# Kernel tuning notes

Measured on AMD Instinct MI355X. Metric: run time of the kernel, lower is better.

Reference implementation:

```python
import jax, jax.numpy as jnp
import numpy as np

LEAKY_SLOPE = 0.2
EPS = 1e-16


def setup_inputs() -> dict:
    key = jax.random.key(0)
    k1, k2, k3, k4, k5 = jax.random.split(key, 5)
    N, E, IN, H, C = 50000, 800000, 128, 4, 16
    x = jax.random.normal(k1, (N, IN), dtype=jnp.float32)
    edge_index = jax.random.randint(k2, (2, E), 0, N, dtype=jnp.int64)
    # xavier_uniform-ish init, gain folded in as plain normal scale for a correctness baseline
    W = jax.random.normal(k3, (IN, H * C), dtype=jnp.float32) * (1.414 * (6.0 / (IN + H * C)) ** 0.5)
    a_src = jax.random.normal(k4, (1, H, C), dtype=jnp.float32) * 0.3
    a_dst = jax.random.normal(k5, (1, H, C), dtype=jnp.float32) * 0.3
    bias = jnp.zeros((H * C,), dtype=jnp.float32)
    return {"x": x, "edge_index": edge_index, "W": W, "a_src": a_src, "a_dst": a_dst, "bias": bias}


def reference(x, edge_index, W, a_src, a_dst, bias):
    N = x.shape[0]
    H, C = a_src.shape[1], a_src.shape[2]
    h = (x @ W).reshape(N, H, C)                      # [N, H, C]
    src, dst = edge_index[0], edge_index[1]
    alpha_src = (h * a_src).sum(-1)                    # [N, H]
    alpha_dst = (h * a_dst).sum(-1)                    # [N, H]
    alpha = alpha_src[src] + alpha_dst[dst]            # [E, H]
    alpha = jnp.where(alpha >= 0, alpha, LEAKY_SLOPE * alpha)
    # segment softmax over edges grouped by dst
    max_per = jax.ops.segment_max(alpha, dst, num_segments=N)  # [N, H], -inf for empty
    max_per = jnp.where(jnp.isinf(max_per), jnp.zeros_like(max_per), max_per)
    exp_s = jnp.exp(alpha - max_per[dst])              # [E, H]
    denom = jax.ops.segment_sum(exp_s, dst, num_segments=N)
    denom = jnp.maximum(denom, EPS)
    attn = exp_s / denom[dst]                          # [E, H]
    msg = h[src] * attn[..., None]                     # [E, H, C]
    out = jax.ops.segment_sum(msg, dst, num_segments=N)  # [N, H, C]
    out = out.reshape(N, H * C) + bias                 # concat=True
    return out
```

## Files before the change

kernel.cpp:

```cpp
#include <hip/hip_runtime.h>

#define LEAKY 0.2f
#define EPSV 1e-16f

constexpr int N_IN = 128;
constexpr int HC   = 64;
constexpr int H    = 4;
constexpr int CAP  = 48;
constexpr int LDK  = 136;
constexpr int SH   = 6;
constexpr int BNODES = 64;
constexpr int NBK  = 782;
constexpr int BCAP = 1344;
constexpr int CHUNK = 2048;

typedef __attribute__((ext_vector_type(8))) short bf16x8;
typedef __attribute__((ext_vector_type(4))) float f32x4;

__device__ __forceinline__ unsigned short bf16_rne(float f) {
    unsigned int b = __float_as_uint(f);
    return (unsigned short)((b + 0x7fffu + ((b >> 16) & 1u)) >> 16);
}

__global__ __launch_bounds__(256) void gemm_bin_fused(
        const float* __restrict__ x,
        const float* __restrict__ W,
        const float* __restrict__ a_src,
        const float* __restrict__ a_dst,
        const int* __restrict__ src,
        const int* __restrict__ dst,
        unsigned short* __restrict__ h_bf,
        float* __restrict__ as_out,
        float* __restrict__ ad_out,
        unsigned int* __restrict__ binned,
        int* __restrict__ bcursor,
        int N, int E, int gb) {
    __shared__ __align__(16) char smem[2 * 64 * LDK * sizeof(unsigned short)];
    int t = threadIdx.x;

    if (blockIdx.x >= gb) {
        int* hist  = (int*)smem;
        int* run   = hist + NBK;
        int* basep = run + NBK;
        for (int i = t; i < NBK; i += 256) { hist[i] = 0; run[i] = 0; }
        __syncthreads();

        int e0 = (blockIdx.x - gb) * CHUNK;
        int myb[8]; unsigned int myv[8];
        #pragma unroll
        for (int i = 0; i < 8; ++i) {
            int e = e0 + i * 256 + t;
            if (e < E) {
                int s = src[e], d = dst[e];
                myb[i] = d >> SH;
                myv[i] = ((unsigned int)(d & (BNODES - 1)) << 16) | (unsigned int)s;
                atomicAdd(&hist[myb[i]], 1);
            } else myb[i] = -1;
        }
        __syncthreads();

        for (int i = t; i < NBK; i += 256) {
            int h = hist[i];
            basep[i] = h ? atomicAdd(&bcursor[i], h) : 0;
        }
        __syncthreads();

        #pragma unroll
        for (int i = 0; i < 8; ++i) {
            int b = myb[i];
            if (b >= 0) {
                int r = atomicAdd(&run[b], 1);
                int g = basep[b] + r;
                if (g < BCAP) binned[b * BCAP + g] = myv[i];
            }
        }
        return;
    }

    unsigned short* xt = (unsigned short*)smem;
    unsigned short* wt = xt + 64 * LDK;
    int rowbase_blk = blockIdx.x * 64;

    #pragma unroll
    for (int i = 0; i < 32; ++i) {
        int idx = i * 256 + t;
        int k = idx >> 6, c = idx & 63;
        wt[c * LDK + k] = bf16_rne(W[idx]);
    }

    #pragma unroll
    for (int i = 0; i < 8; ++i) {
        int f = i * 256 + t;
        int row = f >> 5;
        int f4  = f & 31;
        int g = rowbase_blk + row;
        float4 v = (g < N) ? ((const float4*)x)[(size_t)g * 32 + f4]
                           : make_float4(0.f, 0.f, 0.f, 0.f);
        ushort4 pv;
        pv.x = bf16_rne(v.x); pv.y = bf16_rne(v.y);
        pv.z = bf16_rne(v.z); pv.w = bf16_rne(v.w);
        *(ushort4*)&xt[row * LDK + f4 * 4] = pv;
    }
    __syncthreads();

    int w = t >> 6, l = t & 63;
    int cl = l & 15;
    int rg = (l >> 4) * 4;

    f32x4 acc[4] = {{0,0,0,0},{0,0,0,0},{0,0,0,0},{0,0,0,0}};

    const int arow = w * 16 + cl;
    const int koff = (l >> 4) * 8;
    #pragma unroll
    for (int kk = 0; kk < 4; ++kk) {
        bf16x8 af = *(const bf16x8*)&xt[arow * LDK + kk * 32 + koff];
        #pragma unroll
        for (int c = 0; c < 4; ++c) {
            bf16x8 bfr = *(const bf16x8*)&wt[(c * 16 + cl) * LDK + kk * 32 + koff];
            acc[c] = __builtin_amdgcn_mfma_f32_16x16x32_bf16(af, bfr, acc[c], 0, 0, 0);
        }
    }

    float asv[4], adv[4];
    #pragma unroll
    for (int c = 0; c < 4; ++c) {
        asv[c] = a_src[c * 16 + cl];
        adv[c] = a_dst[c * 16 + cl];
    }

    float as_rc[4][4], ad_rc[4][4];
    #pragma unroll
    for (int c = 0; c < 4; ++c) {
        #pragma unroll
        for (int r = 0; r < 4; ++r) {
            float v = acc[c][r];
            int g = rowbase_blk + w * 16 + rg + r;
            if (g < N) h_bf[(size_t)g * HC + c * 16 + cl] = bf16_rne(v);
            as_rc[r][c] = v * asv[c];
            ad_rc[r][c] = v * adv[c];
        }
    }

    #pragma unroll
    for (int off = 1; off < 16; off <<= 1) {
        #pragma unroll
        for (int r = 0; r < 4; ++r)
            #pragma unroll
            for (int c = 0; c < 4; ++c) {
                as_rc[r][c] += __shfl_xor(as_rc[r][c], off, 64);
                ad_rc[r][c] += __shfl_xor(ad_rc[r][c], off, 64);
            }
    }

    #pragma unroll
    for (int r = 0; r < 4; ++r)
        #pragma unroll
        for (int c = 0; c < 4; ++c) {
            if (cl == r * 4 + c) {
                int g = rowbase_blk + w * 16 + rg + r;
                if (g < N) {
                    as_out[g * H + c] = as_rc[r][c];
                    ad_out[g * H + c] = ad_rc[r][c];
                }
            }
        }
}

__global__ __launch_bounds__(512) void agg_fused(
        const unsigned int* __restrict__ binned, const int* __restrict__ bcursor,
        const unsigned short* __restrict__ h_bf,
        const float* __restrict__ as_in, const float* __restrict__ ad_in,
        const float* __restrict__ bias,
        float* __restrict__ out, int N) {
    __shared__ int cnt[BNODES];
    __shared__ unsigned short lists[BNODES * CAP];
    int b = blockIdx.x, t = threadIdx.x;
    if (t < BNODES) cnt[t] = 0;
    __syncthreads();

    int ne = min(bcursor[b], BCAP);
    const unsigned int* bp = binned + (size_t)b * BCAP;
    for (int i = t; i < ne; i += 512) {
        unsigned int p = bp[i];
        int dl = p >> 16;
        int s  = p & 0xffff;
        int r = atomicAdd(&cnt[dl], 1);
        if (r < CAP) lists[dl * CAP + r] = (unsigned short)s;
    }
    __syncthreads();

    int dl = t >> 3;
    int l8 = t & 7;
    int hh = l8 >> 1;
    const uint4* hp4 = (const uint4*)h_bf;

    int wid = b * BNODES + dl;
    if (wid >= N) return;

    float4 bvlo = ((const float4*)bias)[2 * l8];
    float4 bvhi = ((const float4*)bias)[2 * l8 + 1];

    int deg = min(cnt[dl], CAP);
    float ad_d = ad_in[wid * H + hh];

    float a0 = 0.f, a1 = 0.f, a2 = 0.f, a3 = 0.f;
    float a4 = 0.f, a5 = 0.f, a6 = 0.f, a7 = 0.f;
    float dn = 0.f;

    for (int j = 0; j < deg; j += 4) {
        int ss[4]; float aa[4]; uint4 hv[4];
        #pragma unroll
        for (int k = 0; k < 4; ++k)
            ss[k] = (j + k < deg) ? (int)lists[dl * CAP + j + k] : 0;
        #pragma unroll
        for (int k = 0; k < 4; ++k) {
            aa[k] = as_in[ss[k] * H + hh];
            hv[k] = hp4[(size_t)ss[k] * 8 + l8];
        }
        #pragma unroll
        for (int k = 0; k < 4; ++k) {
            float a = aa[k] + ad_d;
            a = (a >= 0.f) ? a : LEAKY * a;
            float wgt = ((j + k) < deg) ? __expf(a) : 0.f;
            dn += wgt;
            a0 = fmaf(wgt, __uint_as_float(hv[k].x << 16),          a0);
            a1 = fmaf(wgt, __uint_as_float(hv[k].x & 0xffff0000u), a1);
            a2 = fmaf(wgt, __uint_as_float(hv[k].y << 16),          a2);
            a3 = fmaf(wgt, __uint_as_float(hv[k].y & 0xffff0000u), a3);
            a4 = fmaf(wgt, __uint_as_float(hv[k].z << 16),          a4);
            a5 = fmaf(wgt, __uint_as_float(hv[k].z & 0xffff0000u), a5);
            a6 = fmaf(wgt, __uint_as_float(hv[k].w << 16),          a6);
            a7 = fmaf(wgt, __uint_as_float(hv[k].w & 0xffff0000u), a7);
        }
    }

    float inv = 1.f / fmaxf(dn, EPSV);
    float4 olo, ohi;
    olo.x = a0 * inv + bvlo.x;
    olo.y = a1 * inv + bvlo.y;
    olo.z = a2 * inv + bvlo.z;
    olo.w = a3 * inv + bvlo.w;
    ohi.x = a4 * inv + bvhi.x;
    ohi.y = a5 * inv + bvhi.y;
    ohi.z = a6 * inv + bvhi.z;
    ohi.w = a7 * inv + bvhi.w;
    ((float4*)out)[(size_t)wid * 16 + 2 * l8]     = olo;
    ((float4*)out)[(size_t)wid * 16 + 2 * l8 + 1] = ohi;
}

extern "C" void kernel_launch(void* const* d_in, const int* in_sizes, int n_in,
                              void* d_out, int out_size, void* d_ws, size_t ws_size,
                              hipStream_t stream) {
    const float* x     = (const float*)d_in[0];
    const int*   ei    = (const int*)d_in[1];
    const float* W     = (const float*)d_in[2];
    const float* a_src = (const float*)d_in[3];
    const float* a_dst = (const float*)d_in[4];
    const float* bias  = (const float*)d_in[5];

    int N = in_sizes[0] / N_IN;
    int E = in_sizes[1] / 2;
    const int* src = ei;
    const int* dst = ei + E;

    float* out = (float*)d_out;

    unsigned short* h_bf = (unsigned short*)d_ws;
    float* as_buf = (float*)(h_bf + (size_t)N * HC);
    float* ad_buf = as_buf + (size_t)N * H;
    unsigned int* binned = (unsigned int*)(ad_buf + (size_t)N * H);
    int* bcursor  = (int*)(binned + (size_t)NBK * BCAP);

    hipMemsetAsync(bcursor, 0, NBK * sizeof(int), stream);

    int gb = (N + 63) / 64;
    int bb = (E + CHUNK - 1) / CHUNK;
    gemm_bin_fused<<<gb + bb, 256, 0, stream>>>(
        x, W, a_src, a_dst, src, dst, h_bf, as_buf, ad_buf, binned, bcursor, N, E, gb);

    agg_fused<<<NBK, 512, 0, stream>>>(
        binned, bcursor, h_bf, as_buf, ad_buf, bias, out, N);
}
```

Measured before the change: 54.40 us.

## Replace global atomic bin cursors with per-chunk local sort and offset table

The edge binning pass no longer reserves slots in fixed-capacity global bins through global atomics. Each chunk block now prefix-scans its local histogram, sorts its edges by bucket into shared memory, writes them out contiguously, and records per-bucket offsets in a transposed table. The aggregation kernel then gathers each bucket's edges by having one thread walk each chunk's slice. This removes the memset, the global atomics and the BCAP overflow truncation. In exchange the agg kernel makes about 391 small serial scattered reads per block, which may be slower than the old contiguous bin read.

```diff
diff --git a/kernel.cpp b/kernel.cpp
--- a/kernel.cpp
+++ b/kernel.cpp
@@ -11,7 +11,7 @@
 constexpr int SH   = 6;
 constexpr int BNODES = 64;
 constexpr int NBK  = 782;
-constexpr int BCAP = 1344;
+constexpr int NBK1 = 783;
 constexpr int CHUNK = 2048;
 
 typedef __attribute__((ext_vector_type(8))) short bf16x8;
@@ -33,19 +33,24 @@
         float* __restrict__ as_out,
         float* __restrict__ ad_out,
         unsigned int* __restrict__ binned,
-        int* __restrict__ bcursor,
+        unsigned short* __restrict__ offT,
         int N, int E, int gb) {
     __shared__ __align__(16) char smem[2 * 64 * LDK * sizeof(unsigned short)];
     int t = threadIdx.x;
 
     if (blockIdx.x >= gb) {
-        int* hist  = (int*)smem;
-        int* run   = hist + NBK;
-        int* basep = run + NBK;
-        for (int i = t; i < NBK; i += 256) { hist[i] = 0; run[i] = 0; }
-        __syncthreads();
-
-        int e0 = (blockIdx.x - gb) * CHUNK;
+        int* hist = (int*)smem;
+        int* pref = hist + 1024;
+        int* run  = pref + 1024;
+        int* wsum = run + 784;
+        unsigned int* stage = (unsigned int*)(wsum + 256);
+
+        for (int i = t; i < 1024; i += 256) { hist[i] = 0; pref[i] = 0; }
+        for (int i = t; i < 784; i += 256) run[i] = 0;
+        __syncthreads();
+
+        int blk = blockIdx.x - gb;
+        int e0 = blk * CHUNK;
         int myb[8]; unsigned int myv[8];
         #pragma unroll
         for (int i = 0; i < 8; ++i) {
@@ -59,21 +64,42 @@
         }
         __syncthreads();
 
-        for (int i = t; i < NBK; i += 256) {
-            int h = hist[i];
-            basep[i] = h ? atomicAdd(&bcursor[i], h) : 0;
-        }
-        __syncthreads();
+        int s4 = 0;
+        #pragma unroll
+        for (int j = 0; j < 4; ++j) s4 += hist[t * 4 + j];
+        wsum[t] = s4;
+        for (int off = 1; off < 256; off <<= 1) {
+            __syncthreads();
+            int add = (t >= off) ? wsum[t - off] : 0;
+            __syncthreads();
+            wsum[t] += add;
+        }
+        __syncthreads();
+        int running = wsum[t] - s4;
+        #pragma unroll
+        for (int j = 0; j < 4; ++j) {
+            int e = t * 4 + j;
+            if (e < NBK1) pref[e] = running;
+            running += hist[e];
+        }
+        __syncthreads();
+
+        for (int e = t; e < NBK1; e += 256)
+            offT[(size_t)blk * NBK1 + e] = (unsigned short)pref[e];
 
         #pragma unroll
         for (int i = 0; i < 8; ++i) {
             int b = myb[i];
             if (b >= 0) {
                 int r = atomicAdd(&run[b], 1);
-                int g = basep[b] + r;
-                if (g < BCAP) binned[b * BCAP + g] = myv[i];
+                stage[pref[b] + r] = myv[i];
             }
         }
+        __syncthreads();
+
+        int nE = min(CHUNK, E - e0);
+        for (int j = t; j < nE; j += 256)
+            binned[(size_t)blk * CHUNK + j] = stage[j];
         return;
     }
 
@@ -167,7 +193,8 @@
 }
 
 __global__ __launch_bounds__(512) void agg_fused(
-        const unsigned int* __restrict__ binned, const int* __restrict__ bcursor,
+        const unsigned int* __restrict__ binned,
+        const unsigned short* __restrict__ offT, int nblk,
         const unsigned short* __restrict__ h_bf,
         const float* __restrict__ as_in, const float* __restrict__ ad_in,
         const float* __restrict__ bias,
@@ -178,14 +205,17 @@
     if (t < BNODES) cnt[t] = 0;
     __syncthreads();
 
-    int ne = min(bcursor[b], BCAP);
-    const unsigned int* bp = binned + (size_t)b * BCAP;
-    for (int i = t; i < ne; i += 512) {
-        unsigned int p = bp[i];
-        int dl = p >> 16;
-        int s  = p & 0xffff;
-        int r = atomicAdd(&cnt[dl], 1);
-        if (r < CAP) lists[dl * CAP + r] = (unsigned short)s;
+    if (t < nblk) {
+        int o0 = offT[(size_t)t * NBK1 + b];
+        int o1 = offT[(size_t)t * NBK1 + b + 1];
+        const unsigned int* bp = binned + (size_t)t * CHUNK;
+        for (int j = o0; j < o1; ++j) {
+            unsigned int p = bp[j];
+            int dl = p >> 16;
+            int s  = p & 0xffff;
+            int r = atomicAdd(&cnt[dl], 1);
+            if (r < CAP) lists[dl * CAP + r] = (unsigned short)s;
+        }
     }
     __syncthreads();
 
@@ -265,19 +295,18 @@
 
     float* out = (float*)d_out;
 
+    int nblk = (E + CHUNK - 1) / CHUNK;
+
     unsigned short* h_bf = (unsigned short*)d_ws;
     float* as_buf = (float*)(h_bf + (size_t)N * HC);
     float* ad_buf = as_buf + (size_t)N * H;
     unsigned int* binned = (unsigned int*)(ad_buf + (size_t)N * H);
-    int* bcursor  = (int*)(binned + (size_t)NBK * BCAP);
-
-    hipMemsetAsync(bcursor, 0, NBK * sizeof(int), stream);
+    unsigned short* offT = (unsigned short*)(binned + (size_t)nblk * CHUNK);
 
     int gb = (N + 63) / 64;
-    int bb = (E + CHUNK - 1) / CHUNK;
-    gemm_bin_fused<<<gb + bb, 256, 0, stream>>>(
-        x, W, a_src, a_dst, src, dst, h_bf, as_buf, ad_buf, binned, bcursor, N, E, gb);
+    gemm_bin_fused<<<gb + nblk, 256, 0, stream>>>(
+        x, W, a_src, a_dst, src, dst, h_bf, as_buf, ad_buf, binned, offT, N, E, gb);
 
     agg_fused<<<NBK, 512, 0, stream>>>(
-        binned, bcursor, h_bf, as_buf, ad_buf, bias, out, N);
+        binned, offT, nblk, h_bf, as_buf, ad_buf, bias, out, N);
 }
```

Measured after the change: 48.82 us (median of 2 runs). 10.3% less time.
